# Kernel optimization log

Measured on AMD Instinct MI355X. Metric: run time of the kernel, lower is better.

The kernel has to match this reference:

```python
import jax, jax.numpy as jnp
from jax import lax
import numpy as np

NEG = -1e30  # log(0) stand-in, finite for NaN-safe grads


def setup_inputs() -> dict:
    key = jax.random.key(0)
    k1, k2, k3, k4, k5 = jax.random.split(key, 5)
    B, T, U, V = 8, 128, 64, 512
    trans_acts = jax.random.normal(k1, (B, T, V), dtype=jnp.float32)
    pred_acts = jax.random.normal(k2, (B, U + 1, V), dtype=jnp.float32)
    labels = jax.random.randint(k3, (B, U), 1, V, dtype=jnp.int32)  # avoid blank=0
    act_lens = jax.random.randint(k4, (B,), T // 2, T + 1, dtype=jnp.int32)
    label_lens = jax.random.randint(k5, (B,), U // 2, U + 1, dtype=jnp.int32)
    return {"trans_acts": trans_acts, "pred_acts": pred_acts, "labels": labels,
            "act_lens": act_lens, "label_lens": label_lens}


def _rnnt_costs(trans_acts, pred_acts, labels, act_lens, label_lens, blank=0):
    B, T, V = trans_acts.shape
    U1 = pred_acts.shape[1]
    U = U1 - 1
    # joint log-probs: log_softmax(trans[:,t] + pred[:,u]) -> (B, T, U+1, V)
    lp = jax.nn.log_softmax(trans_acts[:, :, None, :] + pred_acts[:, None, :, :], axis=-1)
    blank_lp = lp[..., blank]  # (B, T, U+1)
    # label emission log-probs: lab_lp[b,t,u] = lp[b,t,u,labels[b,u]], u < U
    idx = jnp.broadcast_to(labels[:, None, :, None].astype(jnp.int32), (B, T, U, 1))
    lab_lp = jnp.take_along_axis(lp[:, :, :U, :], idx, axis=3)[..., 0]  # (B,T,U)
    valid_u = jnp.arange(U)[None, :] < label_lens[:, None]               # (B,U)
    lab_lp = jnp.where(valid_u[:, None, :], lab_lp, NEG)

    # alpha DP over the (T x U+1) lattice, scan over t, scan over u
    alpha0 = jnp.concatenate(
        [jnp.zeros((B, 1), lp.dtype), jnp.cumsum(lab_lp[:, 0, :], axis=1)], axis=1)

    def outer(alpha_prev, inp):
        blank_prev, lab_row = inp          # (B,U+1), (B,U)
        a = alpha_prev + blank_prev        # come-from-below term
        def inner(x, ins):                 # x: (B,), left-to-right over u
            a_u, lab_p = ins
            x = jnp.logaddexp(a_u, x + lab_p)
            return x, x
        _, xs = lax.scan(inner, a[:, 0], (a[:, 1:].T, lab_row.T))  # (U,B)
        alpha = jnp.concatenate([a[:, :1], xs.T], axis=1)
        return alpha, alpha

    xs_in = (jnp.swapaxes(blank_lp[:, :-1], 0, 1), jnp.swapaxes(lab_lp[:, 1:], 0, 1))
    _, alphas_rest = lax.scan(outer, alpha0, xs_in)              # (T-1,B,U+1)
    alphas = jnp.concatenate([alpha0[None], alphas_rest], axis=0)  # (T,B,U+1)

    b_idx = jnp.arange(B)
    t_idx = act_lens - 1
    u_idx = label_lens
    ll = alphas[t_idx, b_idx, u_idx] + blank_lp[b_idx, t_idx, u_idx]
    return -ll  # per-example negative log-likelihood


def reference(trans_acts, pred_acts, labels, act_lens, label_lens):
    costs = _rnnt_costs(trans_acts, pred_acts, labels, act_lens, label_lens, blank=0)
    # size_average=False: module returns the batch-summed cost as a 1-element tensor
    return jnp.sum(costs)[None]
```

## Files before the change

### kernel.cpp

```cpp
#include <hip/hip_runtime.h>

#define NEG2 (-30000.0f)
#define L2E  1.4426950408889634f
#define LN2  0.6931471805599453f

constexpr int B = 8, T = 128, U = 64, U1 = 65, V = 512;
constexpr int PDROWS = 200;
constexpr int PDW = PDROWS * 64;

constexpr int ETH_F = 0;
constexpr int EPH_F = ETH_F + (B * T * V) / 2;
constexpr int MT_F  = EPH_F + (B * U1 * V) / 2;
constexpr int MP_F  = MT_F + B * T;
constexpr int T0_F  = MP_F + B * U1;
constexpr int P0_F  = T0_F + B * T;
constexpr int PL_F  = P0_F + B * U1;
constexpr int C0_F  = PL_F + B * U1;
constexpr int TL_F  = C0_F + B * T;
constexpr int PD_F  = TL_F + (B * T * 64) / 2;

typedef _Float16 half_t;
typedef _Float16 v4h __attribute__((ext_vector_type(4)));
typedef _Float16 v8h __attribute__((ext_vector_type(8)));
typedef float    v4f __attribute__((ext_vector_type(4)));

__device__ __forceinline__ float wave_shr1(float x) {
    int v = __float_as_int(x);
    int r = __builtin_amdgcn_update_dpp(v, v, 0x138, 0xF, 0xF, false);
    return __int_as_float(r);
}

__global__ __launch_bounds__(256) void k_prep(const float* __restrict__ trans,
                                              const float* __restrict__ pred,
                                              const int* __restrict__ labels,
                                              float* __restrict__ ws,
                                              float* __restrict__ out) {
    if (blockIdx.x == 0 && threadIdx.x == 0) out[0] = 0.0f;
    const int wave = (blockIdx.x * blockDim.x + threadIdx.x) >> 6;
    const int lane = threadIdx.x & 63;
    const int nrows_t = B * T;
    const int nrows = nrows_t + B * U1;
    if (wave >= nrows) return;

    const float* src; half_t* dst;
    if (wave < nrows_t) {
        src = trans + (size_t)wave * V;
        dst = (half_t*)(ws + ETH_F) + (size_t)wave * V;
    } else {
        const int r = wave - nrows_t;
        src = pred + (size_t)r * V;
        dst = (half_t*)(ws + EPH_F) + (size_t)r * V;
    }

    const float4 a = ((const float4*)src)[lane];
    const float4 c = ((const float4*)src)[lane + 64];
    float m = fmaxf(fmaxf(fmaxf(a.x, a.y), fmaxf(a.z, a.w)),
                    fmaxf(fmaxf(c.x, c.y), fmaxf(c.z, c.w)));
    #pragma unroll
    for (int off = 32; off >= 1; off >>= 1) m = fmaxf(m, __shfl_xor(m, off));

    v4h h0 = { (half_t)__expf(a.x - m), (half_t)__expf(a.y - m),
               (half_t)__expf(a.z - m), (half_t)__expf(a.w - m) };
    v4h h1 = { (half_t)__expf(c.x - m), (half_t)__expf(c.y - m),
               (half_t)__expf(c.z - m), (half_t)__expf(c.w - m) };
    ((v4h*)dst)[lane]      = h0;
    ((v4h*)dst)[lane + 64] = h1;

    if (wave < nrows_t) {
        const int b = wave >> 7;
        const int lbl = labels[b * U + lane];
        ((half_t*)(ws + TL_F))[(size_t)wave * 64 + lane] = (half_t)src[lbl];
        if (lane == 0) { ws[MT_F + wave] = m; ws[T0_F + wave] = a.x; }
    } else {
        const int r = wave - nrows_t;
        if (lane == 0) {
            const int b = r / U1, u = r % U1;
            ws[MP_F + r] = m; ws[P0_F + r] = a.x;
            if (u < U) ws[PL_F + r] = src[labels[b * U + u]];
        }
    }
}

__global__ __launch_bounds__(256) void k_joint(const int* __restrict__ label_lens,
                                               float* __restrict__ ws) {
    const int lane = threadIdx.x & 63;
    const int wid = blockIdx.x * 4 + (threadIdx.x >> 6);
    const int b = wid / 40, r = wid % 40;
    const int t0 = (r / 5) * 16, u0 = (r % 5) * 16;
    const int n = lane & 15, q = lane >> 4;

    const v8h* A  = (const v8h*)((const half_t*)(ws + ETH_F) + ((size_t)(b * T + t0 + n)) * V);
    const int  uc = (u0 + n <= 64) ? (u0 + n) : 64;
    const v8h* Bp = (const v8h*)((const half_t*)(ws + EPH_F) + ((size_t)(b * U1 + uc)) * V);

    v4f acc = {0.f, 0.f, 0.f, 0.f};
    #pragma unroll
    for (int c = 0; c < 64; c += 4)
        acc = __builtin_amdgcn_mfma_f32_16x16x32_f16(A[c + q], Bp[c + q], acc, 0, 0, 0);

    const int u = u0 + n;
    if (u > 64) return;
    const int ul = label_lens[b];
    const float mp_u = ws[MP_F + b * U1 + u];
    const float pr0  = ws[P0_F + b * U1 + u];
    const bool has_lab = (u < 64);
    const float prl = has_lab ? ws[PL_F + b * U1 + u] : 0.f;
    half_t* PdH = (half_t*)((uint*)(ws + PD_F) + (size_t)b * PDW);
    const half_t* TLh = (const half_t*)(ws + TL_F) + (size_t)(b * T) * 64;

    #pragma unroll
    for (int i = 0; i < 4; ++i) {
        const int t = t0 + q * 4 + i;
        const float mt = ws[MT_F + b * T + t];
        const float lse2 = (mt + mp_u) * L2E + __log2f(acc[i]);
        const float bl2 = (ws[T0_F + b * T + t] + pr0) * L2E - lse2;
        const int d = t + u + 1;
        if (u >= 1) PdH[(d * 64 + (u - 1)) * 2] = (half_t)bl2;
        else        ws[C0_F + b * T + t] = bl2;
        if (has_lab) {
            const float lb2 = (u >= ul) ? NEG2
                             : ((float)TLh[t * 64 + u] + prl) * L2E - lse2;
            PdH[(d * 64 + u) * 2 + 1] = (half_t)lb2;
        }
    }
}

__device__ __forceinline__ float dp_step(float cur, uint w, float a00, int d, int l, int tl) {
    const int t = d - l - 1;
    union { uint u; half_t h[2]; } cv; cv.u = w;
    const float bn = (float)cv.h[0];
    const float lb = (float)cv.h[1];
    const float sh = wave_shr1(cur);
    const float lv = (l == 0) ? a00 : sh;
    const float a2 = lv + lb;
    const float a1 = (t >= 1) ? cur + bn : NEG2;
    const float m  = fmaxf(a1, a2);
    const float nc = m + __log2f(exp2f(a1 - m) + exp2f(a2 - m));
    return ((t >= 0) && (t <= tl)) ? nc : cur;
}

__global__ __launch_bounds__(64) void k_dp(const float* __restrict__ ws,
                                           const int* __restrict__ act_lens,
                                           const int* __restrict__ label_lens,
                                           float* __restrict__ out) {
    const int b = blockIdx.x, l = threadIdx.x;

    constexpr int DROWS = 192;
    __shared__ uint Pds[DROWS * 64];
    __shared__ float af[T];

    const uint4* src4 = (const uint4*)((const uint*)(ws + PD_F) + (size_t)b * PDW + 64);
    uint4* dst4 = (uint4*)Pds;
    #pragma unroll
    for (int i = 0; i < DROWS / 4; ++i)
        dst4[i * 64 + l] = src4[i * 64 + l];

    const float* c0 = ws + C0_F + b * T;
    float x0 = c0[l], x1 = c0[64 + l];
    #pragma unroll
    for (int off = 1; off < 64; off <<= 1) { float y = __shfl_up(x0, off); if (l >= off) x0 += y; }
    #pragma unroll
    for (int off = 1; off < 64; off <<= 1) { float y = __shfl_up(x1, off); if (l >= off) x1 += y; }
    const float tot = __shfl(x0, 63);
    if (l == 0) af[0] = 0.0f;
    af[l + 1] = x0;
    if (l < 63) af[65 + l] = tot + x1;
    __syncthreads();

    const int tl = act_lens[b] - 1;
    const int ul = label_lens[b];
    const int dmax = tl + ul;
    const int steps = (dmax + 3) >> 2;

    uint  w0 = Pds[0 * 64 + l], w1 = Pds[1 * 64 + l], w2 = Pds[2 * 64 + l], w3 = Pds[3 * 64 + l];
    float a0 = af[0], a1 = af[1], a2 = af[2], a3 = af[3];

    float cur = 0.0f;
    int d = 1;
    for (int s = 0; s < steps; ++s) {
        cur = dp_step(cur, w0, a0, d, l, tl);
        w0 = Pds[min(d + 3, DROWS - 1) * 64 + l]; a0 = af[min(d + 3, T - 1)]; ++d;
        cur = dp_step(cur, w1, a1, d, l, tl);
        w1 = Pds[min(d + 3, DROWS - 1) * 64 + l]; a1 = af[min(d + 3, T - 1)]; ++d;
        cur = dp_step(cur, w2, a2, d, l, tl);
        w2 = Pds[min(d + 3, DROWS - 1) * 64 + l]; a2 = af[min(d + 3, T - 1)]; ++d;
        cur = dp_step(cur, w3, a3, d, l, tl);
        w3 = Pds[min(d + 3, DROWS - 1) * 64 + l]; a3 = af[min(d + 3, T - 1)]; ++d;
    }

    if (l == ul - 1) {
        union { uint u; half_t h[2]; } cv; cv.u = Pds[dmax * 64 + (ul - 1)];
        atomicAdd(out, -((cur + (float)cv.h[0]) * LN2));
    }
}

extern "C" void kernel_launch(void* const* d_in, const int* in_sizes, int n_in,
                              void* d_out, int out_size, void* d_ws, size_t ws_size,
                              hipStream_t stream) {
    const float* trans      = (const float*)d_in[0];
    const float* pred       = (const float*)d_in[1];
    const int*   labels     = (const int*)d_in[2];
    const int*   act_lens   = (const int*)d_in[3];
    const int*   label_lens = (const int*)d_in[4];
    float* ws  = (float*)d_ws;
    float* out = (float*)d_out;

    const int nrows = B * T + B * U1;
    k_prep<<<(nrows + 3) / 4, 256, 0, stream>>>(trans, pred, labels, ws, out);
    k_joint<<<80, 256, 0, stream>>>(label_lens, ws);
    k_dp<<<8, 64, 0, stream>>>(ws, act_lens, label_lens, out);
}
```

Baseline: 89.56 us.

## Fuse prep, joint MFMA and DP into one per-batch kernel

Merges the three kernels into a single kernel with one 512-thread block per batch element. Per-row max, label values and the diagonal-ordered log-prob table now stay in shared memory instead of going through the global workspace, and the output is zeroed with a memset. This removes two kernel launches and the global round trips, but only 8 blocks run, so the prep and MFMA phases use a small fraction of the GPU compared with the previous multi-block launches. Shared memory use per block rises to roughly 70 KB.

```diff
diff --git a/kernel.cpp b/kernel.cpp
--- a/kernel.cpp
+++ b/kernel.cpp
@@ -5,20 +5,8 @@
 #define LN2  0.6931471805599453f
 
 constexpr int B = 8, T = 128, U = 64, U1 = 65, V = 512;
-constexpr int PDROWS = 200;
-constexpr int PDW = PDROWS * 64;
 
-constexpr int ETH_F = 0;
-constexpr int EPH_F = ETH_F + (B * T * V) / 2;
-constexpr int MT_F  = EPH_F + (B * U1 * V) / 2;
-constexpr int MP_F  = MT_F + B * T;
-constexpr int T0_F  = MP_F + B * U1;
-constexpr int P0_F  = T0_F + B * T;
-constexpr int PL_F  = P0_F + B * U1;
-constexpr int C0_F  = PL_F + B * U1;
-constexpr int TL_F  = C0_F + B * T;
-constexpr int PD_F  = TL_F + (B * T * 64) / 2;
-
+constexpr size_t ETH_TOT = (size_t)B * T * V;
 typedef _Float16 half_t;
 typedef _Float16 v4h __attribute__((ext_vector_type(4)));
 typedef _Float16 v8h __attribute__((ext_vector_type(8)));
@@ -28,101 +16,6 @@
     int v = __float_as_int(x);
     int r = __builtin_amdgcn_update_dpp(v, v, 0x138, 0xF, 0xF, false);
     return __int_as_float(r);
-}
-
-__global__ __launch_bounds__(256) void k_prep(const float* __restrict__ trans,
-                                              const float* __restrict__ pred,
-                                              const int* __restrict__ labels,
-                                              float* __restrict__ ws,
-                                              float* __restrict__ out) {
-    if (blockIdx.x == 0 && threadIdx.x == 0) out[0] = 0.0f;
-    const int wave = (blockIdx.x * blockDim.x + threadIdx.x) >> 6;
-    const int lane = threadIdx.x & 63;
-    const int nrows_t = B * T;
-    const int nrows = nrows_t + B * U1;
-    if (wave >= nrows) return;
-
-    const float* src; half_t* dst;
-    if (wave < nrows_t) {
-        src = trans + (size_t)wave * V;
-        dst = (half_t*)(ws + ETH_F) + (size_t)wave * V;
-    } else {
-        const int r = wave - nrows_t;
-        src = pred + (size_t)r * V;
-        dst = (half_t*)(ws + EPH_F) + (size_t)r * V;
-    }
-
-    const float4 a = ((const float4*)src)[lane];
-    const float4 c = ((const float4*)src)[lane + 64];
-    float m = fmaxf(fmaxf(fmaxf(a.x, a.y), fmaxf(a.z, a.w)),
-                    fmaxf(fmaxf(c.x, c.y), fmaxf(c.z, c.w)));
-    #pragma unroll
-    for (int off = 32; off >= 1; off >>= 1) m = fmaxf(m, __shfl_xor(m, off));
-
-    v4h h0 = { (half_t)__expf(a.x - m), (half_t)__expf(a.y - m),
-               (half_t)__expf(a.z - m), (half_t)__expf(a.w - m) };
-    v4h h1 = { (half_t)__expf(c.x - m), (half_t)__expf(c.y - m),
-               (half_t)__expf(c.z - m), (half_t)__expf(c.w - m) };
-    ((v4h*)dst)[lane]      = h0;
-    ((v4h*)dst)[lane + 64] = h1;
-
-    if (wave < nrows_t) {
-        const int b = wave >> 7;
-        const int lbl = labels[b * U + lane];
-        ((half_t*)(ws + TL_F))[(size_t)wave * 64 + lane] = (half_t)src[lbl];
-        if (lane == 0) { ws[MT_F + wave] = m; ws[T0_F + wave] = a.x; }
-    } else {
-        const int r = wave - nrows_t;
-        if (lane == 0) {
-            const int b = r / U1, u = r % U1;
-            ws[MP_F + r] = m; ws[P0_F + r] = a.x;
-            if (u < U) ws[PL_F + r] = src[labels[b * U + u]];
-        }
-    }
-}
-
-__global__ __launch_bounds__(256) void k_joint(const int* __restrict__ label_lens,
-                                               float* __restrict__ ws) {
-    const int lane = threadIdx.x & 63;
-    const int wid = blockIdx.x * 4 + (threadIdx.x >> 6);
-    const int b = wid / 40, r = wid % 40;
-    const int t0 = (r / 5) * 16, u0 = (r % 5) * 16;
-    const int n = lane & 15, q = lane >> 4;
-
-    const v8h* A  = (const v8h*)((const half_t*)(ws + ETH_F) + ((size_t)(b * T + t0 + n)) * V);
-    const int  uc = (u0 + n <= 64) ? (u0 + n) : 64;
-    const v8h* Bp = (const v8h*)((const half_t*)(ws + EPH_F) + ((size_t)(b * U1 + uc)) * V);
-
-    v4f acc = {0.f, 0.f, 0.f, 0.f};
-    #pragma unroll
-    for (int c = 0; c < 64; c += 4)
-        acc = __builtin_amdgcn_mfma_f32_16x16x32_f16(A[c + q], Bp[c + q], acc, 0, 0, 0);
-
-    const int u = u0 + n;
-    if (u > 64) return;
-    const int ul = label_lens[b];
-    const float mp_u = ws[MP_F + b * U1 + u];
-    const float pr0  = ws[P0_F + b * U1 + u];
-    const bool has_lab = (u < 64);
-    const float prl = has_lab ? ws[PL_F + b * U1 + u] : 0.f;
-    half_t* PdH = (half_t*)((uint*)(ws + PD_F) + (size_t)b * PDW);
-    const half_t* TLh = (const half_t*)(ws + TL_F) + (size_t)(b * T) * 64;
-
-    #pragma unroll
-    for (int i = 0; i < 4; ++i) {
-        const int t = t0 + q * 4 + i;
-        const float mt = ws[MT_F + b * T + t];
-        const float lse2 = (mt + mp_u) * L2E + __log2f(acc[i]);
-        const float bl2 = (ws[T0_F + b * T + t] + pr0) * L2E - lse2;
-        const int d = t + u + 1;
-        if (u >= 1) PdH[(d * 64 + (u - 1)) * 2] = (half_t)bl2;
-        else        ws[C0_F + b * T + t] = bl2;
-        if (has_lab) {
-            const float lb2 = (u >= ul) ? NEG2
-                             : ((float)TLh[t * 64 + u] + prl) * L2E - lse2;
-            PdH[(d * 64 + u) * 2 + 1] = (half_t)lb2;
-        }
-    }
 }
 
 __device__ __forceinline__ float dp_step(float cur, uint w, float a00, int d, int l, int tl) {
@@ -139,24 +32,107 @@
     return ((t >= 0) && (t <= tl)) ? nc : cur;
 }
 
-__global__ __launch_bounds__(64) void k_dp(const float* __restrict__ ws,
-                                           const int* __restrict__ act_lens,
-                                           const int* __restrict__ label_lens,
-                                           float* __restrict__ out) {
-    const int b = blockIdx.x, l = threadIdx.x;
+__global__ __launch_bounds__(512) void k_fused(const float* __restrict__ trans,
+                                               const float* __restrict__ pred,
+                                               const int* __restrict__ labels,
+                                               const int* __restrict__ act_lens,
+                                               const int* __restrict__ label_lens,
+                                               float* __restrict__ ws,
+                                               float* __restrict__ out) {
+    const int b   = blockIdx.x;
+    const int tid = threadIdx.x;
+    const int wid = tid >> 6;
+    const int l   = tid & 63;
 
-    constexpr int DROWS = 192;
-    __shared__ uint Pds[DROWS * 64];
-    __shared__ float af[T];
+    __shared__ uint   Pds[192 * 64];
+    __shared__ float  af[T];
+    __shared__ float  C0[T];
+    __shared__ float  MT[T], T0[T];
+    __shared__ float  MP[U1], P0[U1], PL[U1];
+    __shared__ half_t TL[T * 64];
 
-    const uint4* src4 = (const uint4*)((const uint*)(ws + PD_F) + (size_t)b * PDW + 64);
-    uint4* dst4 = (uint4*)Pds;
-    #pragma unroll
-    for (int i = 0; i < DROWS / 4; ++i)
-        dst4[i * 64 + l] = src4[i * 64 + l];
+    half_t* wsh  = (half_t*)ws;
+    half_t* ethb = wsh + (size_t)b * T * V;
+    half_t* ephb = wsh + ETH_TOT + (size_t)b * U1 * V;
 
-    const float* c0 = ws + C0_F + b * T;
-    float x0 = c0[l], x1 = c0[64 + l];
+    const int ul = label_lens[b];
+    const int tl = act_lens[b] - 1;
+    const int mylbl = labels[b * U + l];
+
+    for (int r = wid; r < T + U1; r += 8) {
+        const float* src; half_t* dst;
+        if (r < T) { src = trans + ((size_t)b * T + r) * V;        dst = ethb + (size_t)r * V; }
+        else       { src = pred  + ((size_t)b * U1 + (r - T)) * V; dst = ephb + (size_t)(r - T) * V; }
+
+        const float4 a = ((const float4*)src)[l];
+        const float4 c = ((const float4*)src)[l + 64];
+        float m = fmaxf(fmaxf(fmaxf(a.x, a.y), fmaxf(a.z, a.w)),
+                        fmaxf(fmaxf(c.x, c.y), fmaxf(c.z, c.w)));
+        #pragma unroll
+        for (int off = 32; off >= 1; off >>= 1) m = fmaxf(m, __shfl_xor(m, off));
+
+        v4h h0 = { (half_t)__expf(a.x - m), (half_t)__expf(a.y - m),
+                   (half_t)__expf(a.z - m), (half_t)__expf(a.w - m) };
+        v4h h1 = { (half_t)__expf(c.x - m), (half_t)__expf(c.y - m),
+                   (half_t)__expf(c.z - m), (half_t)__expf(c.w - m) };
+        ((v4h*)dst)[l]      = h0;
+        ((v4h*)dst)[l + 64] = h1;
+
+        if (r < T) {
+            TL[r * 64 + l] = (half_t)src[mylbl];
+            if (l == 0) { MT[r] = m; T0[r] = a.x; }
+        } else {
+            const int u = r - T;
+            if (l == 0) {
+                MP[u] = m; P0[u] = a.x;
+                if (u < U) PL[u] = src[labels[b * U + u]];
+            }
+        }
+    }
+    __threadfence_block();
+    __syncthreads();
+
+    {
+        const int n = l & 15, q = l >> 4;
+        const int t0 = wid * 16;
+        const v8h* A = (const v8h*)(ethb + (size_t)(t0 + n) * V);
+        #pragma unroll 1
+        for (int ut = 0; ut < 5; ++ut) {
+            const int u0 = ut * 16;
+            const int uc = (u0 + n <= 64) ? (u0 + n) : 64;
+            const v8h* Bp = (const v8h*)(ephb + (size_t)uc * V);
+
+            v4f acc = {0.f, 0.f, 0.f, 0.f};
+            #pragma unroll
+            for (int c = 0; c < 64; c += 4)
+                acc = __builtin_amdgcn_mfma_f32_16x16x32_f16(A[c + q], Bp[c + q], acc, 0, 0, 0);
+
+            const int u = u0 + n;
+            if (u > 64) continue;
+            const float mp_u = MP[u], pr0 = P0[u];
+            const bool has_lab = (u < 64);
+            const float prl = has_lab ? PL[u] : 0.f;
+            #pragma unroll
+            for (int i = 0; i < 4; ++i) {
+                const int t = t0 + q * 4 + i;
+                const float lse2 = (MT[t] + mp_u) * L2E + __log2f(acc[i]);
+                const float bl2 = (T0[t] + pr0) * L2E - lse2;
+                const int row = t + u;
+                if (u >= 1) ((half_t*)&Pds[row * 64 + (u - 1)])[0] = (half_t)bl2;
+                else        C0[t] = bl2;
+                if (has_lab) {
+                    const float lb2 = (u >= ul) ? NEG2
+                                     : ((float)TL[t * 64 + u] + prl) * L2E - lse2;
+                    ((half_t*)&Pds[row * 64 + u])[1] = (half_t)lb2;
+                }
+            }
+        }
+    }
+    __syncthreads();
+
+    if (wid != 0) return;
+
+    float x0 = C0[l], x1 = C0[64 + l];
     #pragma unroll
     for (int off = 1; off < 64; off <<= 1) { float y = __shfl_up(x0, off); if (l >= off) x0 += y; }
     #pragma unroll
@@ -165,10 +141,7 @@
     if (l == 0) af[0] = 0.0f;
     af[l + 1] = x0;
     if (l < 63) af[65 + l] = tot + x1;
-    __syncthreads();
 
-    const int tl = act_lens[b] - 1;
-    const int ul = label_lens[b];
     const int dmax = tl + ul;
     const int steps = (dmax + 3) >> 2;
 
@@ -179,13 +152,13 @@
     int d = 1;
     for (int s = 0; s < steps; ++s) {
         cur = dp_step(cur, w0, a0, d, l, tl);
-        w0 = Pds[min(d + 3, DROWS - 1) * 64 + l]; a0 = af[min(d + 3, T - 1)]; ++d;
+        w0 = Pds[min(d + 3, 191) * 64 + l]; a0 = af[min(d + 3, T - 1)]; ++d;
         cur = dp_step(cur, w1, a1, d, l, tl);
-        w1 = Pds[min(d + 3, DROWS - 1) * 64 + l]; a1 = af[min(d + 3, T - 1)]; ++d;
+        w1 = Pds[min(d + 3, 191) * 64 + l]; a1 = af[min(d + 3, T - 1)]; ++d;
         cur = dp_step(cur, w2, a2, d, l, tl);
-        w2 = Pds[min(d + 3, DROWS - 1) * 64 + l]; a2 = af[min(d + 3, T - 1)]; ++d;
+        w2 = Pds[min(d + 3, 191) * 64 + l]; a2 = af[min(d + 3, T - 1)]; ++d;
         cur = dp_step(cur, w3, a3, d, l, tl);
-        w3 = Pds[min(d + 3, DROWS - 1) * 64 + l]; a3 = af[min(d + 3, T - 1)]; ++d;
+        w3 = Pds[min(d + 3, 191) * 64 + l]; a3 = af[min(d + 3, T - 1)]; ++d;
     }
 
     if (l == ul - 1) {
@@ -205,8 +178,6 @@
     float* ws  = (float*)d_ws;
     float* out = (float*)d_out;
 
-    const int nrows = B * T + B * U1;
-    k_prep<<<(nrows + 3) / 4, 256, 0, stream>>>(trans, pred, labels, ws, out);
-    k_joint<<<80, 256, 0, stream>>>(label_lens, ws);
-    k_dp<<<8, 64, 0, stream>>>(ws, act_lens, label_lens, out);
+    hipMemsetAsync(out, 0, sizeof(float), stream);
+    k_fused<<<B, 512, 0, stream>>>(trans, pred, labels, act_lens, label_lens, ws, out);
 }
```

Measured after the change: 124.4 us. 38.9% more time.

## Fuse softmax-exp prep into joint MFMA kernel, dropping fp16 workspace staging

Applied to the files above, without the earlier changes.

Removes the separate prep kernel and has each joint wave read the fp32 trans/pred rows directly, compute row maxima, exponentiate into fp16 on the fly and feed MFMA. This drops one kernel launch and the round-trip of the fp16 exp tables, row stats and label gathers through global workspace. The cost is redundant work: each trans row is reduced and exponentiated once per u-tile (5x) and each pred row once per t-tile (8x), and the reads are fp32 instead of fp16.

```diff
diff --git a/kernel.cpp b/kernel.cpp
--- a/kernel.cpp
+++ b/kernel.cpp
@@ -8,19 +8,10 @@
 constexpr int PDROWS = 200;
 constexpr int PDW = PDROWS * 64;
 
-constexpr int ETH_F = 0;
-constexpr int EPH_F = ETH_F + (B * T * V) / 2;
-constexpr int MT_F  = EPH_F + (B * U1 * V) / 2;
-constexpr int MP_F  = MT_F + B * T;
-constexpr int T0_F  = MP_F + B * U1;
-constexpr int P0_F  = T0_F + B * T;
-constexpr int PL_F  = P0_F + B * U1;
-constexpr int C0_F  = PL_F + B * U1;
-constexpr int TL_F  = C0_F + B * T;
-constexpr int PD_F  = TL_F + (B * T * 64) / 2;
+constexpr int C0_F = 0;
+constexpr int PD_F = C0_F + B * T;
 
 typedef _Float16 half_t;
-typedef _Float16 v4h __attribute__((ext_vector_type(4)));
 typedef _Float16 v8h __attribute__((ext_vector_type(8)));
 typedef float    v4f __attribute__((ext_vector_type(4)));
 
@@ -28,101 +19,6 @@
     int v = __float_as_int(x);
     int r = __builtin_amdgcn_update_dpp(v, v, 0x138, 0xF, 0xF, false);
     return __int_as_float(r);
-}
-
-__global__ __launch_bounds__(256) void k_prep(const float* __restrict__ trans,
-                                              const float* __restrict__ pred,
-                                              const int* __restrict__ labels,
-                                              float* __restrict__ ws,
-                                              float* __restrict__ out) {
-    if (blockIdx.x == 0 && threadIdx.x == 0) out[0] = 0.0f;
-    const int wave = (blockIdx.x * blockDim.x + threadIdx.x) >> 6;
-    const int lane = threadIdx.x & 63;
-    const int nrows_t = B * T;
-    const int nrows = nrows_t + B * U1;
-    if (wave >= nrows) return;
-
-    const float* src; half_t* dst;
-    if (wave < nrows_t) {
-        src = trans + (size_t)wave * V;
-        dst = (half_t*)(ws + ETH_F) + (size_t)wave * V;
-    } else {
-        const int r = wave - nrows_t;
-        src = pred + (size_t)r * V;
-        dst = (half_t*)(ws + EPH_F) + (size_t)r * V;
-    }
-
-    const float4 a = ((const float4*)src)[lane];
-    const float4 c = ((const float4*)src)[lane + 64];
-    float m = fmaxf(fmaxf(fmaxf(a.x, a.y), fmaxf(a.z, a.w)),
-                    fmaxf(fmaxf(c.x, c.y), fmaxf(c.z, c.w)));
-    #pragma unroll
-    for (int off = 32; off >= 1; off >>= 1) m = fmaxf(m, __shfl_xor(m, off));
-
-    v4h h0 = { (half_t)__expf(a.x - m), (half_t)__expf(a.y - m),
-               (half_t)__expf(a.z - m), (half_t)__expf(a.w - m) };
-    v4h h1 = { (half_t)__expf(c.x - m), (half_t)__expf(c.y - m),
-               (half_t)__expf(c.z - m), (half_t)__expf(c.w - m) };
-    ((v4h*)dst)[lane]      = h0;
-    ((v4h*)dst)[lane + 64] = h1;
-
-    if (wave < nrows_t) {
-        const int b = wave >> 7;
-        const int lbl = labels[b * U + lane];
-        ((half_t*)(ws + TL_F))[(size_t)wave * 64 + lane] = (half_t)src[lbl];
-        if (lane == 0) { ws[MT_F + wave] = m; ws[T0_F + wave] = a.x; }
-    } else {
-        const int r = wave - nrows_t;
-        if (lane == 0) {
-            const int b = r / U1, u = r % U1;
-            ws[MP_F + r] = m; ws[P0_F + r] = a.x;
-            if (u < U) ws[PL_F + r] = src[labels[b * U + u]];
-        }
-    }
-}
-
-__global__ __launch_bounds__(256) void k_joint(const int* __restrict__ label_lens,
-                                               float* __restrict__ ws) {
-    const int lane = threadIdx.x & 63;
-    const int wid = blockIdx.x * 4 + (threadIdx.x >> 6);
-    const int b = wid / 40, r = wid % 40;
-    const int t0 = (r / 5) * 16, u0 = (r % 5) * 16;
-    const int n = lane & 15, q = lane >> 4;
-
-    const v8h* A  = (const v8h*)((const half_t*)(ws + ETH_F) + ((size_t)(b * T + t0 + n)) * V);
-    const int  uc = (u0 + n <= 64) ? (u0 + n) : 64;
-    const v8h* Bp = (const v8h*)((const half_t*)(ws + EPH_F) + ((size_t)(b * U1 + uc)) * V);
-
-    v4f acc = {0.f, 0.f, 0.f, 0.f};
-    #pragma unroll
-    for (int c = 0; c < 64; c += 4)
-        acc = __builtin_amdgcn_mfma_f32_16x16x32_f16(A[c + q], Bp[c + q], acc, 0, 0, 0);
-
-    const int u = u0 + n;
-    if (u > 64) return;
-    const int ul = label_lens[b];
-    const float mp_u = ws[MP_F + b * U1 + u];
-    const float pr0  = ws[P0_F + b * U1 + u];
-    const bool has_lab = (u < 64);
-    const float prl = has_lab ? ws[PL_F + b * U1 + u] : 0.f;
-    half_t* PdH = (half_t*)((uint*)(ws + PD_F) + (size_t)b * PDW);
-    const half_t* TLh = (const half_t*)(ws + TL_F) + (size_t)(b * T) * 64;
-
-    #pragma unroll
-    for (int i = 0; i < 4; ++i) {
-        const int t = t0 + q * 4 + i;
-        const float mt = ws[MT_F + b * T + t];
-        const float lse2 = (mt + mp_u) * L2E + __log2f(acc[i]);
-        const float bl2 = (ws[T0_F + b * T + t] + pr0) * L2E - lse2;
-        const int d = t + u + 1;
-        if (u >= 1) PdH[(d * 64 + (u - 1)) * 2] = (half_t)bl2;
-        else        ws[C0_F + b * T + t] = bl2;
-        if (has_lab) {
-            const float lb2 = (u >= ul) ? NEG2
-                             : ((float)TLh[t * 64 + u] + prl) * L2E - lse2;
-            PdH[(d * 64 + u) * 2 + 1] = (half_t)lb2;
-        }
-    }
 }
 
 __device__ __forceinline__ float dp_step(float cur, uint w, float a00, int d, int l, int tl) {
@@ -137,6 +33,88 @@
     const float m  = fmaxf(a1, a2);
     const float nc = m + __log2f(exp2f(a1 - m) + exp2f(a2 - m));
     return ((t >= 0) && (t <= tl)) ? nc : cur;
+}
+
+__global__ __launch_bounds__(256, 1) void k_joint(const float* __restrict__ trans,
+                                                  const float* __restrict__ pred,
+                                                  const int* __restrict__ labels,
+                                                  const int* __restrict__ label_lens,
+                                                  float* __restrict__ ws,
+                                                  float* __restrict__ out) {
+    if (blockIdx.x == 0 && threadIdx.x == 0) out[0] = 0.0f;
+
+    const int wid = threadIdx.x >> 6, l = threadIdx.x & 63;
+    const int n = l & 15, q = l >> 4;
+    const int b    = blockIdx.x / 10;
+    const int task = (blockIdx.x % 10) * 4 + wid;
+    const int t0 = (task / 5) * 16, u0 = (task % 5) * 16;
+
+    __shared__ float SMT[4][16], ST0[4][16], SMP[4][16], SP0[4][16], SPL[4][16];
+
+    const float*  Arow = trans + ((size_t)b * T + t0 + n) * V;
+    const int     ur   = (u0 + n <= 64) ? (u0 + n) : 64;
+    const float*  Brow = pred + ((size_t)b * U1 + ur) * V;
+    const float4* A4 = (const float4*)Arow;
+    const float4* B4 = (const float4*)Brow;
+
+    float mA = -1e30f, mB = -1e30f, a0x = 0.f, b0x = 0.f;
+    #pragma unroll 16
+    for (int i = 0; i < 32; ++i) {
+        const float4 va = A4[q * 32 + i];
+        const float4 vb = B4[q * 32 + i];
+        if (i == 0 && q == 0) { a0x = va.x; b0x = vb.x; }
+        mA = fmaxf(mA, fmaxf(fmaxf(va.x, va.y), fmaxf(va.z, va.w)));
+        mB = fmaxf(mB, fmaxf(fmaxf(vb.x, vb.y), fmaxf(vb.z, vb.w)));
+    }
+    mA = fmaxf(mA, __shfl_xor(mA, 16)); mA = fmaxf(mA, __shfl_xor(mA, 32));
+    mB = fmaxf(mB, __shfl_xor(mB, 16)); mB = fmaxf(mB, __shfl_xor(mB, 32));
+
+    if (q == 0) {
+        SMT[wid][n] = mA; ST0[wid][n] = a0x;
+        SMP[wid][n] = mB; SP0[wid][n] = b0x;
+        SPL[wid][n] = (u0 + n < U) ? Brow[labels[b * U + u0 + n]] : 0.f;
+    }
+
+    v4f acc = {0.f, 0.f, 0.f, 0.f};
+    #pragma unroll 4
+    for (int s = 0; s < 16; ++s) {
+        const float4 fa0 = A4[s * 8 + q * 2], fa1 = A4[s * 8 + q * 2 + 1];
+        const float4 fb0 = B4[s * 8 + q * 2], fb1 = B4[s * 8 + q * 2 + 1];
+        const v8h Af = { (half_t)__expf(fa0.x - mA), (half_t)__expf(fa0.y - mA),
+                         (half_t)__expf(fa0.z - mA), (half_t)__expf(fa0.w - mA),
+                         (half_t)__expf(fa1.x - mA), (half_t)__expf(fa1.y - mA),
+                         (half_t)__expf(fa1.z - mA), (half_t)__expf(fa1.w - mA) };
+        const v8h Bf = { (half_t)__expf(fb0.x - mB), (half_t)__expf(fb0.y - mB),
+                         (half_t)__expf(fb0.z - mB), (half_t)__expf(fb0.w - mB),
+                         (half_t)__expf(fb1.x - mB), (half_t)__expf(fb1.y - mB),
+                         (half_t)__expf(fb1.z - mB), (half_t)__expf(fb1.w - mB) };
+        acc = __builtin_amdgcn_mfma_f32_16x16x32_f16(Af, Bf, acc, 0, 0, 0);
+    }
+
+    const int u = u0 + n;
+    if (u > 64) return;
+    const int ul = label_lens[b];
+    const float mp_u = SMP[wid][n], pr0 = SP0[wid][n];
+    const bool has_lab = (u < U);
+    const float prl = has_lab ? SPL[wid][n] : 0.f;
+    const int lblu = has_lab ? labels[b * U + u] : 0;
+    half_t* PdH = (half_t*)((uint*)(ws + PD_F) + (size_t)b * PDW);
+
+    #pragma unroll
+    for (int i = 0; i < 4; ++i) {
+        const int t = t0 + q * 4 + i;
+        const float mt = SMT[wid][q * 4 + i];
+        const float lse2 = (mt + mp_u) * L2E + __log2f(acc[i]);
+        const float bl2 = (ST0[wid][q * 4 + i] + pr0) * L2E - lse2;
+        const int d = t + u + 1;
+        if (u >= 1) PdH[(d * 64 + (u - 1)) * 2] = (half_t)bl2;
+        else        ws[C0_F + b * T + t] = bl2;
+        if (has_lab) {
+            const float lb2 = (u >= ul) ? NEG2
+                             : (trans[((size_t)b * T + t) * V + lblu] + prl) * L2E - lse2;
+            PdH[(d * 64 + u) * 2 + 1] = (half_t)lb2;
+        }
+    }
 }
 
 __global__ __launch_bounds__(64) void k_dp(const float* __restrict__ ws,
@@ -205,8 +183,6 @@
     float* ws  = (float*)d_ws;
     float* out = (float*)d_out;
 
-    const int nrows = B * T + B * U1;
-    k_prep<<<(nrows + 3) / 4, 256, 0, stream>>>(trans, pred, labels, ws, out);
-    k_joint<<<80, 256, 0, stream>>>(label_lens, ws);
+    k_joint<<<80, 256, 0, stream>>>(trans, pred, labels, label_lens, ws, out);
     k_dp<<<8, 64, 0, stream>>>(ws, act_lens, label_lens, out);
 }
```

New measurement: 98.39 us. 1.1x slower.
